# Kernel optimization log

Hardware: AMD Instinct MI355X
Metric: run time of the kernel (lower is better)

The kernel has to match this reference:

```python
import jax, jax.numpy as jnp
import numpy as np

B, S, QW, HID, HEADS = 1, 4096, 512, 512, 8
D = HID // HEADS  # size_per_head = 64
SCALE = 1.0 / np.sqrt(float(D))


def setup_inputs() -> dict:
    key = jax.random.key(0)
    k1, k2, k3, k4, k5 = jax.random.split(key, 5)
    return {
        "tensor_q": jax.random.normal(k1, (B, S, QW), dtype=jnp.float32),
        "tensor_k": jax.random.normal(k2, (B, S, QW), dtype=jnp.float32),
        "tensor_v": jax.random.normal(k3, (B, S, QW), dtype=jnp.float32),
        # in_proj_layer: [3*hidden, q_width] (torch uses rand uniform init; randn fine for reference)
        "in_proj": jax.random.normal(k4, (3 * HID, QW), dtype=jnp.float32) * 0.02,
        # out_proj: nn.Linear(hidden, out, bias=False) weight shape [out, hidden]
        "w_out": jax.random.normal(k5, (HID, HID), dtype=jnp.float32) * 0.02,
    }


def reference(tensor_q, tensor_k, tensor_v, in_proj, w_out):
    b, s, _ = tensor_q.shape
    wq, wk, wv = in_proj[:HID], in_proj[HID:2 * HID], in_proj[2 * HID:]
    # mm(W, x_2d^T)^T  ==  x_2d @ W^T ; reshape to [b, s, heads, d]
    q = (tensor_q.reshape(-1, QW) @ wq.T).reshape(b, s, HEADS, D)
    k = (tensor_k.reshape(-1, QW) @ wk.T).reshape(b, s, HEADS, D)
    v = (tensor_v.reshape(-1, QW) @ wv.T).reshape(b, s, HEADS, D)
    # scores: [b, h, s_q, s_k], explicitly materialized as in the source
    scores = jnp.einsum('bqhd,bkhd->bhqk', q, k) * SCALE
    probs = jax.nn.softmax(scores, axis=-1)
    ctx = jnp.einsum('bhqk,bkhd->bqhd', probs, v).reshape(b * s, HID)
    out = ctx @ w_out.T
    return out.reshape(b, s, HID)
```

## Files before the change

### kernel.cpp

```cpp
#include <hip/hip_runtime.h>
#include <hip/hip_bf16.h>

#define S_LEN 4096
#define QW_K  512
#define HID_N 512
#define HEADS 8
#define DH    64
#define QSCALE (0.125f * 1.4426950408889634f)

typedef _Float16 f16;
typedef _Float16 half8  __attribute__((ext_vector_type(8)));
typedef _Float16 half4v __attribute__((ext_vector_type(4)));
typedef float    float4v __attribute__((ext_vector_type(4)));
typedef float    f32x16 __attribute__((ext_vector_type(16)));
typedef unsigned int uint;
typedef unsigned int uint4v __attribute__((ext_vector_type(4)));

__device__ inline uint pkh(float a, float b) {
    return __builtin_bit_cast(uint, __builtin_amdgcn_cvt_pkrtz(a, b));
}
__device__ inline void plswap(uint& a, uint& b) {
    asm volatile("v_permlane32_swap_b32 %0, %1" : "+v"(a), "+v"(b));
}
__device__ inline float hexp2(float x) {
    float r;
    asm("v_exp_f32 %0, %1" : "=v"(r) : "v"(x));
    return r;
}


__global__ __launch_bounds__(256) void proj_kernel(
    const float* __restrict__ xq, const float* __restrict__ xk,
    const float* __restrict__ xv, const float* __restrict__ in_proj,
    f16* __restrict__ qws, f16* __restrict__ kws, f16* __restrict__ vtws)
{
    __shared__ f16 As[128][40];
    __shared__ f16 Ws[128][40];

    const int tid  = threadIdx.x;
    const int lane = tid & 63;
    const int w    = tid >> 6;
    const int wm   = w >> 1, wn = w & 1;
    const int l15  = lane & 15, g = lane >> 4;
    const int m0   = blockIdx.x * 128;
    const int n0   = blockIdx.y * 128;
    const int matid = n0 >> 9;
    const float* A = (matid == 0) ? xq : (matid == 1) ? xk : xv;

    float4v acc[4][4];
    for (int i = 0; i < 4; i++)
        for (int j = 0; j < 4; j++)
            for (int r = 0; r < 4; r++) acc[i][j][r] = 0.0f;

    const int srow = tid >> 3;
    const int scol = (tid & 7) * 4;

    for (int k0 = 0; k0 < QW_K; k0 += 32) {
        __syncthreads();
        #pragma unroll
        for (int p = 0; p < 4; p++) {
            int r = p * 32 + srow;
            float4v av = *(const float4v*)(A + (size_t)(m0 + r) * QW_K + k0 + scol);
            float4v wv = *(const float4v*)(in_proj + (size_t)(n0 + r) * QW_K + k0 + scol);
            half4v ah, wh;
            for (int e = 0; e < 4; e++) { ah[e] = (f16)av[e]; wh[e] = (f16)wv[e]; }
            *(half4v*)&As[r][scol] = ah;
            *(half4v*)&Ws[r][scol] = wh;
        }
        __syncthreads();

        half8 a[4], b[4];
        #pragma unroll
        for (int i = 0; i < 4; i++) a[i] = *(const half8*)&As[wm * 64 + i * 16 + l15][g * 8];
        #pragma unroll
        for (int j = 0; j < 4; j++) b[j] = *(const half8*)&Ws[wn * 64 + j * 16 + l15][g * 8];
        #pragma unroll
        for (int i = 0; i < 4; i++)
            #pragma unroll
            for (int j = 0; j < 4; j++)
                acc[i][j] = __builtin_amdgcn_mfma_f32_16x16x32_f16(a[i], b[j], acc[i][j], 0, 0, 0);
    }

    #pragma unroll
    for (int i = 0; i < 4; i++) {
        int grow0 = m0 + wm * 64 + i * 16 + g * 4;
        #pragma unroll
        for (int j = 0; j < 4; j++) {
            int gcol = n0 + wn * 64 + j * 16 + l15;
            int c = gcol & 511;
            int h = c >> 6, d = c & 63;
            if (matid == 2) {
                int db = d >> 5, l31v = d & 31;
                int kb16 = grow0 >> 4;
                int g5v  = (grow0 >> 3) & 1;
                int e0   = grow0 & 7;
                half4v pv;
                for (int r = 0; r < 4; r++) pv[r] = (f16)acc[i][j][r];
                *(half4v*)(vtws + ((size_t)((h * 2 + db) * 256 + kb16) << 9)
                                + l31v * 16 + g5v * 8 + e0) = pv;
            } else if (matid == 0) {
                for (int r = 0; r < 4; r++)
                    qws[((size_t)h * S_LEN + grow0 + r) * DH + d] = (f16)(acc[i][j][r] * QSCALE);
            } else {
                int dblk = d >> 4, g5k = (d >> 3) & 1, e = d & 7;
                for (int r = 0; r < 4; r++) {
                    int s = grow0 + r;
                    kws[((size_t)((h * 128 + (s >> 5)) * 4 + dblk) << 9)
                        + (s & 31) * 16 + g5k * 8 + e] = (f16)acc[i][j][r];
                }
            }
        }
    }
}

__global__ __launch_bounds__(256) void attn_kernel(
    const f16* __restrict__ qws, const f16* __restrict__ kws,
    const f16* __restrict__ vtws, float* __restrict__ ctx0,
    float* __restrict__ ctx1, float* __restrict__ L0, float* __restrict__ L1)
{
    __shared__ f16 Kl[8][512];
    __shared__ f16 Vl[8][512];

    const int tid  = threadIdx.x;
    const int lane = tid & 63;
    const int w    = tid >> 6;
    const int l31  = lane & 31;
    const int g5   = lane >> 5;
    const int blk  = blockIdx.x;
    const int kvh  = blk >> 8;
    const int h    = blk & 7;
    const int qb   = (blk >> 3) & 31;
    const int q0   = qb * 128 + w * 32;

    const f16* Kf = kws  + (((size_t)h * 512) << 9);
    const f16* Vf = vtws + (((size_t)h * 512) << 9);
    const int pw = ((lane & 1) * 32 + (lane >> 1)) * 8;

    half8 qf[4];
    {
        const f16* qp = qws + ((size_t)h * S_LEN + q0 + l31) * DH + g5 * 8;
        #pragma unroll
        for (int dblk = 0; dblk < 4; dblk++)
            qf[dblk] = *(const half8*)(qp + dblk * 16);
    }

    float lsum = 0.0f;
    f32x16 oacc0, oacc1;
    #pragma unroll
    for (int i = 0; i < 16; i++) { oacc0[i] = 0.0f; oacc1[i] = 0.0f; }

    const int c0 = w * 2;
    const int T0 = kvh * 32;
    half8 kst[2], vst[2];
    #pragma unroll
    for (int i = 0; i < 2; i++) {
        const int c = c0 + i;
        kst[i] = *(const half8*)(Kf
            + ((size_t)((T0 * 2 + (c >> 2)) * 4 + (c & 3)) << 9) + lane * 8);
        vst[i] = *(const half8*)(Vf
            + ((size_t)(((c >> 2) << 8) + T0 * 4 + (c & 3)) << 9) + lane * 8);
    }

    for (int t = 0; t < 32; t++) {
        __syncthreads();
        #pragma unroll
        for (int i = 0; i < 2; i++) {
            *(half8*)&Kl[c0 + i][pw] = kst[i];
            *(half8*)&Vl[c0 + i][pw] = vst[i];
        }
        if (t + 1 < 32) {
            const int T = T0 + t + 1;
            #pragma unroll
            for (int i = 0; i < 2; i++) {
                const int c = c0 + i;
                kst[i] = *(const half8*)(Kf
                    + ((size_t)((T * 2 + (c >> 2)) * 4 + (c & 3)) << 9) + lane * 8);
                vst[i] = *(const half8*)(Vf
                    + ((size_t)(((c >> 2) << 8) + T * 4 + (c & 3)) << 9) + lane * 8);
            }
        }
        __syncthreads();

        half8 kf0[4], kf1[4], vf0[4], vf1[4];
        #pragma unroll
        for (int d = 0; d < 4; d++) {
            kf0[d] = *(const half8*)&Kl[d][lane * 8];
            kf1[d] = *(const half8*)&Kl[4 + d][lane * 8];
        }
        #pragma unroll
        for (int k = 0; k < 4; k++) {
            vf0[k] = *(const half8*)&Vl[k][lane * 8];
            vf1[k] = *(const half8*)&Vl[4 + k][lane * 8];
        }

        f32x16 st0, st1;
        #pragma unroll
        for (int i = 0; i < 16; i++) { st0[i] = 0.0f; st1[i] = 0.0f; }
        __builtin_amdgcn_s_setprio(1);
        #pragma unroll
        for (int dblk = 0; dblk < 4; dblk++) {
            st0 = __builtin_amdgcn_mfma_f32_32x32x16_f16(kf0[dblk], qf[dblk], st0, 0, 0, 0);
            st1 = __builtin_amdgcn_mfma_f32_32x32x16_f16(kf1[dblk], qf[dblk], st1, 0, 0, 0);
        }
        __builtin_amdgcn_s_setprio(0);

        #pragma unroll
        for (int i = 0; i < 16; i++) {
            st0[i] = hexp2(st0[i]);
            st1[i] = hexp2(st1[i]);
        }

        f32x16 ss;
        #pragma unroll
        for (int i = 0; i < 16; i++) ss[i] = st0[i] + st1[i];
        #pragma unroll
        for (int off = 8; off >= 1; off >>= 1)
            #pragma unroll
            for (int i = 0; i < off; i++) ss[i] += ss[i + off];
        lsum += ss[0];

        half8 pf[4];
        #pragma unroll
        for (int kb = 0; kb < 2; kb++) {
            uint w0 = pkh(st0[8 * kb + 0], st0[8 * kb + 1]);
            uint w1 = pkh(st0[8 * kb + 2], st0[8 * kb + 3]);
            uint w2 = pkh(st0[8 * kb + 4], st0[8 * kb + 5]);
            uint w3 = pkh(st0[8 * kb + 6], st0[8 * kb + 7]);
            plswap(w0, w2);
            plswap(w1, w3);
            uint4v u; u[0] = w0; u[1] = w1; u[2] = w2; u[3] = w3;
            pf[kb] = __builtin_bit_cast(half8, u);
        }
        #pragma unroll
        for (int kb = 0; kb < 2; kb++) {
            uint w0 = pkh(st1[8 * kb + 0], st1[8 * kb + 1]);
            uint w1 = pkh(st1[8 * kb + 2], st1[8 * kb + 3]);
            uint w2 = pkh(st1[8 * kb + 4], st1[8 * kb + 5]);
            uint w3 = pkh(st1[8 * kb + 6], st1[8 * kb + 7]);
            plswap(w0, w2);
            plswap(w1, w3);
            uint4v u; u[0] = w0; u[1] = w1; u[2] = w2; u[3] = w3;
            pf[2 + kb] = __builtin_bit_cast(half8, u);
        }

        __builtin_amdgcn_s_setprio(1);
        #pragma unroll
        for (int kb = 0; kb < 4; kb++) {
            oacc0 = __builtin_amdgcn_mfma_f32_32x32x16_f16(vf0[kb], pf[kb], oacc0, 0, 0, 0);
            oacc1 = __builtin_amdgcn_mfma_f32_32x32x16_f16(vf1[kb], pf[kb], oacc1, 0, 0, 0);
        }
        __builtin_amdgcn_s_setprio(0);
    }

    lsum += __shfl_xor(lsum, 32);
    float* cx = kvh ? ctx1 : ctx0;
    float* Lx = kvh ? L1 : L0;
    float* cbase = cx + (size_t)(q0 + l31) * HID_N + h * DH;
    #pragma unroll
    for (int rg = 0; rg < 4; rg++) {
        float4v v0, v1;
        #pragma unroll
        for (int j = 0; j < 4; j++) {
            v0[j] = oacc0[rg * 4 + j];
            v1[j] = oacc1[rg * 4 + j];
        }
        const int dd = rg * 8 + g5 * 4;
        *(float4v*)(cbase + dd)      = v0;
        *(float4v*)(cbase + 32 + dd) = v1;
    }
    if (g5 == 0) Lx[(q0 + l31) * 8 + h] = lsum;
}

__global__ __launch_bounds__(256) void outproj_kernel(
    const float* __restrict__ ctx0, const float* __restrict__ ctx1,
    const float* __restrict__ L0, const float* __restrict__ L1,
    const float* __restrict__ w_out, float* __restrict__ out)
{
    __shared__ f16 As[128][40];
    __shared__ f16 Ws[128][40];

    const int tid  = threadIdx.x;
    const int lane = tid & 63;
    const int w    = tid >> 6;
    const int wm   = w >> 1, wn = w & 1;
    const int l15  = lane & 15, g = lane >> 4;
    const int m0   = blockIdx.x * 128;
    const int n0   = blockIdx.y * 128;

    float4v acc[4][4];
    for (int i = 0; i < 4; i++)
        for (int j = 0; j < 4; j++)
            for (int r = 0; r < 4; r++) acc[i][j][r] = 0.0f;

    const int srow = tid >> 3;
    const int scol = (tid & 7) * 4;

    for (int k0 = 0; k0 < HID_N; k0 += 32) {
        __syncthreads();
        const int hh = (k0 + scol) >> 6;
        #pragma unroll
        for (int p = 0; p < 4; p++) {
            int r = p * 32 + srow;
            int s = m0 + r;
            float4v a0 = *(const float4v*)(ctx0 + (size_t)s * HID_N + k0 + scol);
            float4v a1 = *(const float4v*)(ctx1 + (size_t)s * HID_N + k0 + scol);
            float inv = 1.0f / (L0[s * 8 + hh] + L1[s * 8 + hh]);
            float4v wv = *(const float4v*)(w_out + (size_t)(n0 + r) * HID_N + k0 + scol);
            half4v ah, wh;
            for (int e = 0; e < 4; e++) {
                ah[e] = (f16)((a0[e] + a1[e]) * inv);
                wh[e] = (f16)wv[e];
            }
            *(half4v*)&As[r][scol] = ah;
            *(half4v*)&Ws[r][scol] = wh;
        }
        __syncthreads();

        half8 a[4], b[4];
        #pragma unroll
        for (int i = 0; i < 4; i++) a[i] = *(const half8*)&As[wm * 64 + i * 16 + l15][g * 8];
        #pragma unroll
        for (int j = 0; j < 4; j++) b[j] = *(const half8*)&Ws[wn * 64 + j * 16 + l15][g * 8];
        #pragma unroll
        for (int i = 0; i < 4; i++)
            #pragma unroll
            for (int j = 0; j < 4; j++)
                acc[i][j] = __builtin_amdgcn_mfma_f32_16x16x32_f16(a[i], b[j], acc[i][j], 0, 0, 0);
    }

    #pragma unroll
    for (int i = 0; i < 4; i++) {
        int grow0 = m0 + wm * 64 + i * 16 + g * 4;
        #pragma unroll
        for (int j = 0; j < 4; j++) {
            int gcol = n0 + wn * 64 + j * 16 + l15;
            for (int r = 0; r < 4; r++)
                out[(size_t)(grow0 + r) * HID_N + gcol] = acc[i][j][r];
        }
    }
}

extern "C" void kernel_launch(void* const* d_in, const int* in_sizes, int n_in,
                              void* d_out, int out_size, void* d_ws, size_t ws_size,
                              hipStream_t stream)
{
    const float* xq      = (const float*)d_in[0];
    const float* xk      = (const float*)d_in[1];
    const float* xv      = (const float*)d_in[2];
    const float* in_proj = (const float*)d_in[3];
    const float* w_out   = (const float*)d_in[4];
    float* out = (float*)d_out;

    const size_t per = (size_t)HEADS * S_LEN * DH;
    f16* qws   = (f16*)d_ws;
    f16* kws   = qws + per;
    f16* vtws  = kws + per;
    float* ctx0 = (float*)(vtws + per);
    float* ctx1 = ctx0 + (size_t)S_LEN * HID_N;
    float* L0   = ctx1 + (size_t)S_LEN * HID_N;
    float* L1   = L0 + (size_t)S_LEN * HEADS;

    proj_kernel<<<dim3(32, 12), 256, 0, stream>>>(xq, xk, xv, in_proj, qws, kws, vtws);
    attn_kernel<<<dim3(512), 256, 0, stream>>>(qws, kws, vtws, ctx0, ctx1, L0, L1);
    outproj_kernel<<<dim3(32, 4), 256, 0, stream>>>(ctx0, ctx1, L0, L1, w_out, out);
}
```

Measured before the change: 101.0 us.

## Double-buffer K/V LDS tiles with a single barrier per iteration

Turns the single K/V shared-memory tile into a two-stage ping-pong buffer. The next tile is written to the alternate buffer after the MFMAs, so each iteration needs one barrier instead of two. The permuted write index moves from the LDS store to the global read offset, so stores use a linear lane*8 layout. This doubles LDS use per block, which may lower occupancy, and relies on a hand-written waitcnt plus raw barrier being correct.

```diff
diff --git a/kernel.cpp b/kernel.cpp
--- a/kernel.cpp
+++ b/kernel.cpp
@@ -118,8 +118,8 @@
     const f16* __restrict__ vtws, float* __restrict__ ctx0,
     float* __restrict__ ctx1, float* __restrict__ L0, float* __restrict__ L1)
 {
-    __shared__ f16 Kl[8][512];
-    __shared__ f16 Vl[8][512];
+    __shared__ f16 Kl[2][8][512];
+    __shared__ f16 Vl[2][8][512];
 
     const int tid  = threadIdx.x;
     const int lane = tid & 63;
@@ -134,7 +134,7 @@
 
     const f16* Kf = kws  + (((size_t)h * 512) << 9);
     const f16* Vf = vtws + (((size_t)h * 512) << 9);
-    const int pw = ((lane & 1) * 32 + (lane >> 1)) * 8;
+    const int go = (2 * l31 + g5) * 8;
 
     half8 qf[4];
     {
@@ -152,45 +152,39 @@
     const int c0 = w * 2;
     const int T0 = kvh * 32;
     half8 kst[2], vst[2];
+    auto LOADT = [&](int T) {
+        #pragma unroll
+        for (int i = 0; i < 2; i++) {
+            const int c = c0 + i;
+            kst[i] = *(const half8*)(Kf
+                + ((size_t)((T * 2 + (c >> 2)) * 4 + (c & 3)) << 9) + go);
+            vst[i] = *(const half8*)(Vf
+                + ((size_t)(((c >> 2) << 8) + T * 4 + (c & 3)) << 9) + go);
+        }
+    };
+
+    LOADT(T0);
     #pragma unroll
     for (int i = 0; i < 2; i++) {
-        const int c = c0 + i;
-        kst[i] = *(const half8*)(Kf
-            + ((size_t)((T0 * 2 + (c >> 2)) * 4 + (c & 3)) << 9) + lane * 8);
-        vst[i] = *(const half8*)(Vf
-            + ((size_t)(((c >> 2) << 8) + T0 * 4 + (c & 3)) << 9) + lane * 8);
-    }
+        *(half8*)&Kl[0][c0 + i][lane * 8] = kst[i];
+        *(half8*)&Vl[0][c0 + i][lane * 8] = vst[i];
+    }
+    __syncthreads();
+    LOADT(T0 + 1);
 
     for (int t = 0; t < 32; t++) {
-        __syncthreads();
-        #pragma unroll
-        for (int i = 0; i < 2; i++) {
-            *(half8*)&Kl[c0 + i][pw] = kst[i];
-            *(half8*)&Vl[c0 + i][pw] = vst[i];
-        }
-        if (t + 1 < 32) {
-            const int T = T0 + t + 1;
-            #pragma unroll
-            for (int i = 0; i < 2; i++) {
-                const int c = c0 + i;
-                kst[i] = *(const half8*)(Kf
-                    + ((size_t)((T * 2 + (c >> 2)) * 4 + (c & 3)) << 9) + lane * 8);
-                vst[i] = *(const half8*)(Vf
-                    + ((size_t)(((c >> 2) << 8) + T * 4 + (c & 3)) << 9) + lane * 8);
-            }
-        }
-        __syncthreads();
+        const int b = t & 1;
 
         half8 kf0[4], kf1[4], vf0[4], vf1[4];
         #pragma unroll
         for (int d = 0; d < 4; d++) {
-            kf0[d] = *(const half8*)&Kl[d][lane * 8];
-            kf1[d] = *(const half8*)&Kl[4 + d][lane * 8];
+            kf0[d] = *(const half8*)&Kl[b][d][lane * 8];
+            kf1[d] = *(const half8*)&Kl[b][4 + d][lane * 8];
         }
         #pragma unroll
         for (int k = 0; k < 4; k++) {
-            vf0[k] = *(const half8*)&Vl[k][lane * 8];
-            vf1[k] = *(const half8*)&Vl[4 + k][lane * 8];
+            vf0[k] = *(const half8*)&Vl[b][k][lane * 8];
+            vf1[k] = *(const half8*)&Vl[b][4 + k][lane * 8];
         }
 
         f32x16 st0, st1;
@@ -250,6 +244,18 @@
             oacc1 = __builtin_amdgcn_mfma_f32_32x32x16_f16(vf1[kb], pf[kb], oacc1, 0, 0, 0);
         }
         __builtin_amdgcn_s_setprio(0);
+
+        if (t + 1 < 32) {
+            #pragma unroll
+            for (int i = 0; i < 2; i++) {
+                *(half8*)&Kl[b ^ 1][c0 + i][lane * 8] = kst[i];
+                *(half8*)&Vl[b ^ 1][c0 + i][lane * 8] = vst[i];
+            }
+            if (t + 2 < 32) LOADT(T0 + t + 2);
+            asm volatile("s_waitcnt lgkmcnt(0)" ::: "memory");
+            __builtin_amdgcn_s_barrier();
+            asm volatile("" ::: "memory");
+        }
     }
 
     lsum += __shfl_xor(lsum, 32);
```

Measured after the change: 101.9 us. Within noise of the previous version (+0.9%).
